# Kernel tuning notes

Hardware: AMD Instinct MI355X
Metric: run time of the kernel (lower is better)

## Reference

```python
import jax, jax.numpy as jnp
import numpy as np

N_HEAD = 16
N_EMBD = 1024


def setup_inputs() -> dict:
    key = jax.random.key(0)
    k1, k2 = jax.random.split(key)
    x = jax.random.normal(k1, (2, 2048, N_EMBD), dtype=jnp.float32)
    # nn.Linear(n_embd, 3*n_embd, bias=False); store as [in, out] for x @ w
    w_qkv = jax.random.normal(k2, (N_EMBD, 3 * N_EMBD), dtype=jnp.float32) * (N_EMBD ** -0.5)
    return {"x": x, "w_qkv": w_qkv}


def reference(x, w_qkv):
    B, T, C = x.shape
    H = N_HEAD
    D = C // H  # head dim
    qkv = x @ w_qkv  # [B, T, 3C]
    q, k, v = jnp.split(qkv, 3, axis=2)
    # [B, T, H, D] -> [B, H, T, D]
    q = q.reshape(B, T, H, D).transpose(0, 2, 1, 3)
    k = k.reshape(B, T, H, D).transpose(0, 2, 1, 3)
    v = v.reshape(B, T, H, D).transpose(0, 2, 1, 3)
    att = jnp.einsum('bhtd,bhsd->bhts', q, k) / np.sqrt(D).astype(np.float32)
    causal = jnp.tril(jnp.ones((T, T), dtype=bool))  # [T, T]
    att = jnp.where(causal, att, -jnp.inf)
    att = jax.nn.softmax(att, axis=-1)
    out = jnp.einsum('bhts,bhsd->bhtd', att, v)  # [B, H, T, D]
    return out.transpose(0, 2, 1, 3).reshape(B, T, C)
```

## Files before the change

### kernel.cpp

```cpp
#include <hip/hip_runtime.h>
#include <hip/hip_bf16.h>

#define BATCH 2
#define SEQ   2048
#define EMBD  1024
#define NHEAD 16
#define HDIM  64
#define N3    3072
#define MTOT  4096
#define KDIM  1024

typedef __attribute__((ext_vector_type(8))) short  short8;
typedef __attribute__((ext_vector_type(4))) short  s16x4;
typedef __attribute__((ext_vector_type(4))) float  f32x4;

__device__ __forceinline__ short f2bfs(float f) {
    return __builtin_bit_cast(short, __float2bfloat16(f));
}

__global__ __launch_bounds__(256) void cast_x_kernel(const float* __restrict__ x,
                                                     short* __restrict__ xb, int n4) {
    int i = blockIdx.x * 256 + threadIdx.x;
    if (i >= n4) return;
    float4 f = reinterpret_cast<const float4*>(x)[i];
    s16x4 o;
    o[0] = f2bfs(f.x); o[1] = f2bfs(f.y);
    o[2] = f2bfs(f.z); o[3] = f2bfs(f.w);
    reinterpret_cast<s16x4*>(xb)[i] = o;
}

__global__ __launch_bounds__(256) void cast_wt_kernel(const float* __restrict__ w,
                                                      short* __restrict__ wt) {
    __shared__ float tile[32][33];
    int n0 = blockIdx.x * 32;
    int k0 = blockIdx.y * 32;
    int tx = threadIdx.x & 31;
    int ty = threadIdx.x >> 5;
#pragma unroll
    for (int i = 0; i < 4; ++i)
        tile[ty + i * 8][tx] = w[(size_t)(k0 + ty + i * 8) * N3 + n0 + tx];
    __syncthreads();
#pragma unroll
    for (int i = 0; i < 4; ++i)
        wt[(size_t)(n0 + ty + i * 8) * KDIM + k0 + tx] = f2bfs(tile[tx][ty + i * 8]);
}

__device__ __forceinline__ void stage_tile(const short* gbase, short* lbase, int tid) {
#pragma unroll
    for (int c = 0; c < 2; ++c) {
        int row = c * 64 + (tid >> 2);
        int chunk = (tid & 3) ^ ((row >> 1) & 3);
        const short* gp = gbase + (size_t)row * KDIM + chunk * 8;
        short* lp = lbase + c * 2048 + tid * 8;
        __builtin_amdgcn_global_load_lds((const __attribute__((address_space(1))) void*)gp,
                                         (__attribute__((address_space(3))) void*)lp,
                                         16, 0, 0);
    }
}

__global__ __launch_bounds__(256) void qkv_gemm_kernel(const short* __restrict__ xb,
                                                       const short* __restrict__ wt,
                                                       short* __restrict__ qb,
                                                       short* __restrict__ kbuf,
                                                       short* __restrict__ vt) {
    __shared__ short lA[2][128 * 32];
    __shared__ short lB[2][128 * 32];

    const int tid  = threadIdx.x;
    const int lane = tid & 63;
    const int wid  = tid >> 6;
    const int wm = wid >> 1, wn = wid & 1;
    const int lid = blockIdx.x;
    const int swz = (lid & 7) * 96 + (lid >> 3);
    const int m0 = (swz / 24) * 128;
    const int n0 = (swz % 24) * 128;

    f32x4 acc[4][4];
#pragma unroll
    for (int i = 0; i < 4; ++i)
#pragma unroll
        for (int j = 0; j < 4; ++j) acc[i][j] = (f32x4){0.f, 0.f, 0.f, 0.f};

    const short* gA = xb + (size_t)m0 * KDIM;
    const short* gB = wt + (size_t)n0 * KDIM;

    stage_tile(gA, lA[0], tid);
    stage_tile(gB, lB[0], tid);

    int cur = 0;
    const int arow = (lane & 15) * 32 + (((lane >> 4) ^ ((lane >> 1) & 3)) * 8);
#pragma unroll 1
    for (int kt = 0; kt < KDIM / 32; ++kt) {
        if (kt + 1 < KDIM / 32) {
            stage_tile(gA + (kt + 1) * 32, lA[cur ^ 1], tid);
            stage_tile(gB + (kt + 1) * 32, lB[cur ^ 1], tid);
            asm volatile("s_waitcnt vmcnt(4)" ::: "memory");
        } else {
            asm volatile("s_waitcnt vmcnt(0)" ::: "memory");
        }
        __builtin_amdgcn_s_barrier();
        __builtin_amdgcn_sched_barrier(0);
        short8 a[4], b[4];
#pragma unroll
        for (int im = 0; im < 4; ++im)
            a[im] = *(const short8*)&lA[cur][(wm * 64 + im * 16) * 32 + arow];
#pragma unroll
        for (int in = 0; in < 4; ++in)
            b[in] = *(const short8*)&lB[cur][(wn * 64 + in * 16) * 32 + arow];
#pragma unroll
        for (int im = 0; im < 4; ++im)
#pragma unroll
            for (int in = 0; in < 4; ++in)
                acc[im][in] = __builtin_amdgcn_mfma_f32_16x16x32_bf16(a[im], b[in], acc[im][in], 0, 0, 0);
        __builtin_amdgcn_sched_barrier(0);
        __builtin_amdgcn_s_barrier();
        cur ^= 1;
    }

#pragma unroll
    for (int im = 0; im < 4; ++im) {
        int t0m = m0 + wm * 64 + im * 16 + (lane >> 4) * 4;
        int b = t0m >> 11;
        int t0 = t0m & 2047;
#pragma unroll
        for (int in = 0; in < 4; ++in) {
            int col = n0 + wn * 64 + in * 16 + (lane & 15);
            int which = col >> 10;
            int h = (col >> 6) & 15;
            int d = col & 63;
            if (which == 2) {
                s16x4 pk;
#pragma unroll
                for (int r = 0; r < 4; ++r) pk[r] = f2bfs(acc[im][in][r]);
                *(s16x4*)&vt[((size_t)(b * NHEAD + h) * HDIM + d) * SEQ + t0] = pk;
            } else {
                short* dst = (which == 0) ? qb : kbuf;
                float sc = (which == 0) ? 0.125f : 1.0f;
#pragma unroll
                for (int r = 0; r < 4; ++r)
                    dst[((size_t)(b * NHEAD + h) * SEQ + t0 + r) * HDIM + d] = f2bfs(acc[im][in][r] * sc);
            }
        }
    }
}

#define KVB 64

__device__ __forceinline__ int swzf(int r) { return (r & 3) ^ (((r >> 2) & 3) << 1); }

__device__ __forceinline__ void stage_kv(const short* kh, const short* vh, int kb,
                                         short* lk, short* lv, int tid) {
    int row = tid >> 3;
    int sch = (tid & 7) ^ swzf(row);
    const short* gk = kh + (size_t)(kb + row) * HDIM + sch * 8;
    __builtin_amdgcn_global_load_lds((const __attribute__((address_space(1))) void*)gk,
                                     (__attribute__((address_space(3))) void*)(lk + tid * 8), 16, 0, 0);
    const short* gv = vh + (size_t)row * SEQ + kb + sch * 8;
    __builtin_amdgcn_global_load_lds((const __attribute__((address_space(1))) void*)gv,
                                     (__attribute__((address_space(3))) void*)(lv + tid * 8), 16, 0, 0);
}

struct AttnState {
    f32x4 o[4];
    float mrun, lrun;
};

__device__ __forceinline__ void compute_tile(const short* lk, const short* lv, int kb,
                                             int qbase, int qrow, int rbase, int hi,
                                             const short8* aQ, const short8& vone,
                                             AttnState& st) {
    const float L2E = 1.4426950408889634f;
    f32x4 s[4];
    __builtin_amdgcn_s_setprio(1);
#pragma unroll
    for (int nb = 0; nb < 4; ++nb) {
        int kidx = (nb & 1) * 32 + (rbase >> 2) * 8 + (nb >> 1) * 4 + (rbase & 3);
        f32x4 a = (f32x4){0.f, 0.f, 0.f, 0.f};
#pragma unroll
        for (int c = 0; c < 2; ++c) {
            int slot2 = (c * 4 + hi) ^ swzf(kidx);
            short8 bK = *(const short8*)&lk[kidx * 64 + slot2 * 8];
            a = __builtin_amdgcn_mfma_f32_16x16x32_bf16(bK, aQ[c], a, 0, 0, 0);
        }
        s[nb] = a;
    }
    __builtin_amdgcn_s_setprio(0);
    if (kb + KVB - 1 > qbase) {
#pragma unroll
        for (int nb = 0; nb < 4; ++nb) {
            int keyb = kb + (nb & 1) * 32 + hi * 8 + (nb >> 1) * 4;
#pragma unroll
            for (int r = 0; r < 4; ++r)
                if (keyb + r > qrow) s[nb][r] = -1e30f;
        }
    }
    float pm = fmaxf(fmaxf(fmaxf(fmaxf(s[0][0], s[0][1]), s[0][2]),
                           fmaxf(fmaxf(s[0][3], s[1][0]), s[1][1])),
                     fmaxf(fmaxf(fmaxf(s[1][2], s[1][3]), s[2][0]),
                           fmaxf(fmaxf(s[2][1], s[2][2]), s[2][3])));
    pm = fmaxf(fmaxf(pm, s[3][0]), fmaxf(fmaxf(s[3][1], s[3][2]), s[3][3]));
    pm = fmaxf(pm, __shfl_xor(pm, 16));
    pm = fmaxf(pm, __shfl_xor(pm, 32));
    if (__any(pm > st.mrun + 8.0f)) {
        float mnew = fmaxf(st.mrun, pm);
        float sf = exp2f((st.mrun - mnew) * L2E);
        st.mrun = mnew;
        st.lrun *= sf;
#pragma unroll
        for (int dt = 0; dt < 4; ++dt)
#pragma unroll
            for (int r = 0; r < 4; ++r) st.o[dt][r] *= sf;
    }
    float mterm = st.mrun * L2E;
    short8 bp[2];
#pragma unroll
    for (int c = 0; c < 2; ++c)
#pragma unroll
        for (int jj = 0; jj < 8; ++jj) {
            float p = exp2f(fmaf(s[c + (jj >> 2) * 2][jj & 3], L2E, -mterm));
            bp[c][jj] = f2bfs(p);
        }
    f32x4 osum = (f32x4){0.f, 0.f, 0.f, 0.f};
    __builtin_amdgcn_s_setprio(1);
#pragma unroll
    for (int dt = 0; dt < 4; ++dt) {
        int d = dt * 16 + rbase;
#pragma unroll
        for (int c = 0; c < 2; ++c) {
            int slot2 = (c * 4 + hi) ^ swzf(d);
            short8 bV = *(const short8*)&lv[d * 64 + slot2 * 8];
            st.o[dt] = __builtin_amdgcn_mfma_f32_16x16x32_bf16(bV, bp[c], st.o[dt], 0, 0, 0);
        }
    }
#pragma unroll
    for (int c = 0; c < 2; ++c)
        osum = __builtin_amdgcn_mfma_f32_16x16x32_bf16(vone, bp[c], osum, 0, 0, 0);
    __builtin_amdgcn_s_setprio(0);
    st.lrun += osum[0];
}

__global__ __launch_bounds__(512) void attn_kernel(const short* __restrict__ q,
                                                   const short* __restrict__ kk,
                                                   const short* __restrict__ vtg,
                                                   float* __restrict__ out) {
    const int tid  = threadIdx.x;
    const int lane = tid & 63;
    const int wid  = tid >> 6;
    const int lid  = blockIdx.x;
    const int xcd  = lid & 7;
    const int v    = lid >> 3;
    const int h4   = v & 3;
    const int ps   = (v >> 2) & 7;
    const int half = v >> 5;
    const int qt   = half ? ps : (15 - ps);
    const int bh   = h4 * 8 + xcd;
    const int rbase = lane & 15;
    const int hi    = lane >> 4;

    const short* qh = q   + (size_t)bh * SEQ * HDIM;
    const short* kh = kk  + (size_t)bh * SEQ * HDIM;
    const short* vh = vtg + (size_t)bh * HDIM * SEQ;

    __shared__ short lK[2][KVB * 64];
    __shared__ short lV[2][KVB * 64];

    short8 vone;
#pragma unroll
    for (int jj = 0; jj < 8; ++jj) vone[jj] = (short)0x3F80;

    const int b = bh >> 4, h = bh & 15;

    const int qbase = qt * 128 + wid * 16;
    const int qrow  = qbase + rbase;

    short8 aQ[2];
#pragma unroll
    for (int c = 0; c < 2; ++c)
        aQ[c] = *(const short8*)&qh[(size_t)qrow * HDIM + c * 32 + hi * 8];

    AttnState st;
#pragma unroll
    for (int i = 0; i < 4; ++i) st.o[i] = (f32x4){0.f, 0.f, 0.f, 0.f};
    st.mrun = -INFINITY;
    st.lrun = 0.f;

    const int ktiles = 2 * qt + 2;
    stage_kv(kh, vh, 0, lK[0], lV[0], tid);
#pragma unroll 1
    for (int t = 0; t < ktiles; t += 2) {
        {
            const int kb = t * KVB;
            if (t + 1 < ktiles) {
                stage_kv(kh, vh, kb + KVB, lK[1], lV[1], tid);
                asm volatile("s_waitcnt vmcnt(2)" ::: "memory");
            } else {
                asm volatile("s_waitcnt vmcnt(0)" ::: "memory");
            }
            __builtin_amdgcn_s_barrier();
            __builtin_amdgcn_sched_barrier(0);
            if (kb < qbase + 16)
                compute_tile(lK[0], lV[0], kb, qbase, qrow, rbase, hi, aQ, vone, st);
            __builtin_amdgcn_sched_barrier(0);
            __builtin_amdgcn_s_barrier();
        }
        if (t + 1 < ktiles) {
            const int kb = (t + 1) * KVB;
            if (t + 2 < ktiles) {
                stage_kv(kh, vh, kb + KVB, lK[0], lV[0], tid);
                asm volatile("s_waitcnt vmcnt(2)" ::: "memory");
            } else {
                asm volatile("s_waitcnt vmcnt(0)" ::: "memory");
            }
            __builtin_amdgcn_s_barrier();
            __builtin_amdgcn_sched_barrier(0);
            if (kb < qbase + 16)
                compute_tile(lK[1], lV[1], kb, qbase, qrow, rbase, hi, aQ, vone, st);
            __builtin_amdgcn_sched_barrier(0);
            __builtin_amdgcn_s_barrier();
        }
    }

    float inv = 1.0f / st.lrun;
#pragma unroll
    for (int dt = 0; dt < 4; ++dt) {
        f32x4 ov;
#pragma unroll
        for (int r = 0; r < 4; ++r) ov[r] = st.o[dt][r] * inv;
        *(f32x4*)&out[((size_t)(b * SEQ + qrow) * NHEAD + h) * HDIM + dt * 16 + hi * 4] = ov;
    }
}

extern "C" void kernel_launch(void* const* d_in, const int* in_sizes, int n_in,
                              void* d_out, int out_size, void* d_ws, size_t ws_size,
                              hipStream_t stream) {
    const float* x = (const float*)d_in[0];
    const float* w = (const float*)d_in[1];
    float* out = (float*)d_out;

    char* ws = (char*)d_ws;
    short* xb   = (short*)(ws);
    short* wt   = (short*)(ws + (size_t)8  * 1024 * 1024);
    short* qb   = (short*)(ws + (size_t)14 * 1024 * 1024);
    short* kbuf = (short*)(ws + (size_t)22 * 1024 * 1024);
    short* vt   = (short*)(ws + (size_t)30 * 1024 * 1024);

    cast_x_kernel<<<dim3(MTOT * KDIM / 4 / 256), dim3(256), 0, stream>>>(x, xb, MTOT * KDIM / 4);
    cast_wt_kernel<<<dim3(N3 / 32, KDIM / 32), dim3(256), 0, stream>>>(w, wt);
    qkv_gemm_kernel<<<dim3(768), dim3(256), 0, stream>>>(xb, wt, qb, kbuf, vt);
    attn_kernel<<<dim3(512), dim3(512), 0, stream>>>(qb, kbuf, vt, out);
}
```

Baseline: 95.73 us.

## Double the attention KV tile to 128 keys with a new V swizzle

Raises the key/value block staged into LDS per iteration from 64 to 128 keys. Staging, the score MFMA loop, masking, softmax packing and the PV MFMAs all change to cover 128 keys, and V gets a wider row layout with a plain XOR swizzle. The aim is to halve the number of loop iterations, barriers and online-softmax rescale checks per query tile. The cost is double the LDS footprint and more registers for scores, which can reduce occupancy, and a launch-bounds minimum-blocks hint is added to keep residency up.

```diff
diff --git a/kernel.cpp b/kernel.cpp
--- a/kernel.cpp
+++ b/kernel.cpp
@@ -144,20 +144,28 @@
     }
 }
 
-#define KVB 64
+#define KVB 128
 
 __device__ __forceinline__ int swzf(int r) { return (r & 3) ^ (((r >> 2) & 3) << 1); }
 
 __device__ __forceinline__ void stage_kv(const short* kh, const short* vh, int kb,
                                          short* lk, short* lv, int tid) {
-    int row = tid >> 3;
-    int sch = (tid & 7) ^ swzf(row);
-    const short* gk = kh + (size_t)(kb + row) * HDIM + sch * 8;
-    __builtin_amdgcn_global_load_lds((const __attribute__((address_space(1))) void*)gk,
-                                     (__attribute__((address_space(3))) void*)(lk + tid * 8), 16, 0, 0);
-    const short* gv = vh + (size_t)row * SEQ + kb + sch * 8;
-    __builtin_amdgcn_global_load_lds((const __attribute__((address_space(1))) void*)gv,
-                                     (__attribute__((address_space(3))) void*)(lv + tid * 8), 16, 0, 0);
+#pragma unroll
+    for (int c = 0; c < 2; ++c) {
+        int row = c * 64 + (tid >> 3);
+        int sch = (tid & 7) ^ swzf(row);
+        const short* gk = kh + (size_t)(kb + row) * HDIM + sch * 8;
+        __builtin_amdgcn_global_load_lds((const __attribute__((address_space(1))) void*)gk,
+                                         (__attribute__((address_space(3))) void*)(lk + c * 4096 + tid * 8), 16, 0, 0);
+    }
+#pragma unroll
+    for (int c = 0; c < 2; ++c) {
+        int d = c * 32 + (tid >> 4);
+        int sch = (tid & 15) ^ (d & 7);
+        const short* gv = vh + (size_t)d * SEQ + kb + sch * 8;
+        __builtin_amdgcn_global_load_lds((const __attribute__((address_space(1))) void*)gv,
+                                         (__attribute__((address_space(3))) void*)(lv + c * 4096 + tid * 8), 16, 0, 0);
+    }
 }
 
 struct AttnState {
@@ -170,11 +178,11 @@
                                              const short8* aQ, const short8& vone,
                                              AttnState& st) {
     const float L2E = 1.4426950408889634f;
-    f32x4 s[4];
+    f32x4 s[8];
     __builtin_amdgcn_s_setprio(1);
 #pragma unroll
-    for (int nb = 0; nb < 4; ++nb) {
-        int kidx = (nb & 1) * 32 + (rbase >> 2) * 8 + (nb >> 1) * 4 + (rbase & 3);
+    for (int nb = 0; nb < 8; ++nb) {
+        int kidx = (nb & 3) * 32 + (rbase >> 2) * 8 + (nb >> 2) * 4 + (rbase & 3);
         f32x4 a = (f32x4){0.f, 0.f, 0.f, 0.f};
 #pragma unroll
         for (int c = 0; c < 2; ++c) {
@@ -187,18 +195,17 @@
     __builtin_amdgcn_s_setprio(0);
     if (kb + KVB - 1 > qbase) {
 #pragma unroll
-        for (int nb = 0; nb < 4; ++nb) {
-            int keyb = kb + (nb & 1) * 32 + hi * 8 + (nb >> 1) * 4;
+        for (int nb = 0; nb < 8; ++nb) {
+            int keyb = kb + (nb & 3) * 32 + hi * 8 + (nb >> 2) * 4;
 #pragma unroll
             for (int r = 0; r < 4; ++r)
                 if (keyb + r > qrow) s[nb][r] = -1e30f;
         }
     }
-    float pm = fmaxf(fmaxf(fmaxf(fmaxf(s[0][0], s[0][1]), s[0][2]),
-                           fmaxf(fmaxf(s[0][3], s[1][0]), s[1][1])),
-                     fmaxf(fmaxf(fmaxf(s[1][2], s[1][3]), s[2][0]),
-                           fmaxf(fmaxf(s[2][1], s[2][2]), s[2][3])));
-    pm = fmaxf(fmaxf(pm, s[3][0]), fmaxf(fmaxf(s[3][1], s[3][2]), s[3][3]));
+    float pm = -INFINITY;
+#pragma unroll
+    for (int nb = 0; nb < 8; ++nb)
+        pm = fmaxf(pm, fmaxf(fmaxf(s[nb][0], s[nb][1]), fmaxf(s[nb][2], s[nb][3])));
     pm = fmaxf(pm, __shfl_xor(pm, 16));
     pm = fmaxf(pm, __shfl_xor(pm, 32));
     if (__any(pm > st.mrun + 8.0f)) {
@@ -212,12 +219,12 @@
             for (int r = 0; r < 4; ++r) st.o[dt][r] *= sf;
     }
     float mterm = st.mrun * L2E;
-    short8 bp[2];
-#pragma unroll
-    for (int c = 0; c < 2; ++c)
+    short8 bp[4];
+#pragma unroll
+    for (int c = 0; c < 4; ++c)
 #pragma unroll
         for (int jj = 0; jj < 8; ++jj) {
-            float p = exp2f(fmaf(s[c + (jj >> 2) * 2][jj & 3], L2E, -mterm));
+            float p = exp2f(fmaf(s[c + (jj >> 2) * 4][jj & 3], L2E, -mterm));
             bp[c][jj] = f2bfs(p);
         }
     f32x4 osum = (f32x4){0.f, 0.f, 0.f, 0.f};
@@ -226,23 +233,23 @@
     for (int dt = 0; dt < 4; ++dt) {
         int d = dt * 16 + rbase;
 #pragma unroll
-        for (int c = 0; c < 2; ++c) {
-            int slot2 = (c * 4 + hi) ^ swzf(d);
-            short8 bV = *(const short8*)&lv[d * 64 + slot2 * 8];
+        for (int c = 0; c < 4; ++c) {
+            int slot2 = (c * 4 + hi) ^ (d & 7);
+            short8 bV = *(const short8*)&lv[d * 128 + slot2 * 8];
             st.o[dt] = __builtin_amdgcn_mfma_f32_16x16x32_bf16(bV, bp[c], st.o[dt], 0, 0, 0);
         }
     }
 #pragma unroll
-    for (int c = 0; c < 2; ++c)
+    for (int c = 0; c < 4; ++c)
         osum = __builtin_amdgcn_mfma_f32_16x16x32_bf16(vone, bp[c], osum, 0, 0, 0);
     __builtin_amdgcn_s_setprio(0);
     st.lrun += osum[0];
 }
 
-__global__ __launch_bounds__(512) void attn_kernel(const short* __restrict__ q,
-                                                   const short* __restrict__ kk,
-                                                   const short* __restrict__ vtg,
-                                                   float* __restrict__ out) {
+__global__ __launch_bounds__(512, 4) void attn_kernel(const short* __restrict__ q,
+                                                      const short* __restrict__ kk,
+                                                      const short* __restrict__ vtg,
+                                                      float* __restrict__ out) {
     const int tid  = threadIdx.x;
     const int lane = tid & 63;
     const int wid  = tid >> 6;
@@ -262,7 +269,7 @@
     const short* vh = vtg + (size_t)bh * HDIM * SEQ;
 
     __shared__ short lK[2][KVB * 64];
-    __shared__ short lV[2][KVB * 64];
+    __shared__ short lV[2][HDIM * KVB];
 
     short8 vone;
 #pragma unroll
@@ -284,7 +291,7 @@
     st.mrun = -INFINITY;
     st.lrun = 0.f;
 
-    const int ktiles = 2 * qt + 2;
+    const int ktiles = qt + 1;
     stage_kv(kh, vh, 0, lK[0], lV[0], tid);
 #pragma unroll 1
     for (int t = 0; t < ktiles; t += 2) {
@@ -292,7 +299,7 @@
             const int kb = t * KVB;
             if (t + 1 < ktiles) {
                 stage_kv(kh, vh, kb + KVB, lK[1], lV[1], tid);
-                asm volatile("s_waitcnt vmcnt(2)" ::: "memory");
+                asm volatile("s_waitcnt vmcnt(4)" ::: "memory");
             } else {
                 asm volatile("s_waitcnt vmcnt(0)" ::: "memory");
             }
@@ -307,7 +314,7 @@
             const int kb = (t + 1) * KVB;
             if (t + 2 < ktiles) {
                 stage_kv(kh, vh, kb + KVB, lK[0], lV[0], tid);
-                asm volatile("s_waitcnt vmcnt(2)" ::: "memory");
+                asm volatile("s_waitcnt vmcnt(4)" ::: "memory");
             } else {
                 asm volatile("s_waitcnt vmcnt(0)" ::: "memory");
             }
```

New measurement: 90.40 us. 1.06x faster.
